# Performance work log

Hardware: AMD Instinct MI355X
Metric: run time of the kernel (lower is better)

## Reference

```python
import jax, jax.numpy as jnp
import numpy as np

N_BLOCKS = 16
BLOCK_SIZE = 512
TOP_K = N_BLOCKS // 4  # matches n_blocks // 4 in the source


def setup_inputs() -> dict:
    key = jax.random.key(0)
    k1, k2, k3, k4, k5 = jax.random.split(key, 5)
    in_f, out_f = 2048, 8192
    x = jax.random.normal(k1, (2, 4096, in_f), dtype=jnp.float32)
    # router: Linear(in_features, n_blocks)
    Wr = jax.random.normal(k2, (N_BLOCKS, in_f), dtype=jnp.float32) * (in_f ** -0.5)
    br = jnp.zeros((N_BLOCKS,), dtype=jnp.float32)
    # fc1: Linear(in, out); fc2: Linear(out, in). Biases are unused in the original forward.
    W1 = jax.random.normal(k3, (out_f, in_f), dtype=jnp.float32) * (in_f ** -0.5)
    W2 = jax.random.normal(k4, (in_f, out_f), dtype=jnp.float32) * (out_f ** -0.5)
    return {"x": x, "Wr": Wr, "br": br, "W1": W1, "W2": W2}


def reference(x, Wr, br, W1, W2):
    x_shape = x.shape
    in_f = x_shape[-1]
    xf = x.reshape(-1, in_f)                      # [N, in]
    n = xf.shape[0]
    # router + top-k block selection per token
    prob = jax.nn.softmax(xf @ Wr.T + br, axis=-1)          # [N, nb]
    _, idx = jax.lax.top_k(prob, TOP_K)                      # [N, k]
    mask = jnp.zeros((n, N_BLOCKS), dtype=xf.dtype)
    mask = mask.at[jnp.arange(n)[:, None], idx].set(1.0)     # [N, nb]
    # fc1 per block: h[n,i,b] = x @ W1_block_i^T  (bias never used in source)
    W1b = W1.reshape(N_BLOCKS, BLOCK_SIZE, in_f)
    h = jnp.einsum('nf,ibf->nib', xf, W1b)                   # [N, nb, bs]
    # activation, then zero out unselected blocks (unselected never reach fc2)
    h = jax.nn.gelu(h, approximate=False) * mask[:, :, None]
    # fc2 per block accumulate: y = sum_i h_i @ W2_block_i^T
    W2b = W2.reshape(in_f, N_BLOCKS, BLOCK_SIZE)
    y = jnp.einsum('nib,fib->nf', h, W2b)                    # [N, in]
    return y.reshape(x_shape)
```

## Files before the change

### kernel.cpp

```cpp
#include <hip/hip_runtime.h>
#include <hip/hip_bf16.h>

#define N_TOK 8192
#define IN_F  2048
#define OUT_F 8192
#define NB    16
#define BS    512
#define BM2   256
#define MAX_MT2 144

typedef short          bf16x8  __attribute__((ext_vector_type(8)));
typedef unsigned short ushort8 __attribute__((ext_vector_type(8)));
typedef float          f32x4   __attribute__((ext_vector_type(4)));
typedef _Float16       f16x8   __attribute__((ext_vector_type(8)));

#define WS_COUNTS 0
#define WS_TSTART 64
#define WS_SEL    256
#define WS_INV    (32*1024)
#define WS_LISTS  (192*1024)
#define WS_XBF    (1ull<<20)
#define WS_W2BF   WS_XBF
#define WS_H      (WS_XBF + 33554432ull)
#define WS_W1BF   (WS_H + 37748736ull)
#define WS_YP     WS_W1BF

static __device__ __forceinline__ unsigned short f2bf(float f) {
    __hip_bfloat16 h = __float2bfloat16(f);
    return *reinterpret_cast<unsigned short*>(&h);
}

static __device__ __forceinline__ void gload16(const unsigned short* g, unsigned short* lds) {
    __builtin_amdgcn_global_load_lds(
        (const __attribute__((address_space(1))) unsigned int*)g,
        (__attribute__((address_space(3))) unsigned int*)lds, 16, 0, 0);
}

__global__ __launch_bounds__(512) void router_kernel(
    const float* __restrict__ x, const float* __restrict__ Wr,
    const float* __restrict__ br, unsigned short* __restrict__ sel,
    unsigned short* __restrict__ x_bf)
{
    __shared__ float xs[8][IN_F];
    __shared__ double logits[8][NB];
    const int tid = threadIdx.x;
    const int lt = tid & 63;
    const int wv = tid >> 6;
    const int tok = blockIdx.x * 8 + wv;
    float4* xl = (float4*)xs[wv];
    const float4* xp = (const float4*)(x + (size_t)tok * IN_F);
    #pragma unroll
    for (int i = 0; i < 8; ++i) xl[lt + i * 64] = xp[lt + i * 64];
    __syncthreads();
    const int e = lt >> 2, p = lt & 3;
    const float4* wp = (const float4*)(Wr + (size_t)e * IN_F);
    double s = 0.0;
    for (int j = p; j < IN_F / 4; j += 4) {
        float4 a = xl[j], w = wp[j];
        s += (double)a.x * w.x + (double)a.y * w.y + (double)a.z * w.z + (double)a.w * w.w;
    }
    s += __shfl_down(s, 2);
    s += __shfl_down(s, 1);
    if (p == 0) logits[wv][e] = s + (double)br[e];
    __syncthreads();
    if (lt == 0) {
        unsigned used = 0, packed = 0;
        #pragma unroll
        for (int kk = 0; kk < 4; ++kk) {
            int best = 0; double bv = -1.0e300;
            #pragma unroll
            for (int i = 0; i < NB; ++i)
                if (!((used >> i) & 1u) && logits[wv][i] > bv) { bv = logits[wv][i]; best = i; }
            used |= 1u << best;
            packed |= (unsigned)best << (4 * kk);
        }
        sel[tok] = (unsigned short)packed;
    }
    const int t7 = tok & 7;
    unsigned short* drow = x_bf + (size_t)tok * IN_F;
    #pragma unroll
    for (int i = 0; i < 4; ++i) {
        const int slot = lt + i * 64;
        const float* sp = &xs[wv][slot * 8];
        ushort8 o;
        #pragma unroll
        for (int j = 0; j < 8; ++j) o[j] = f2bf(sp[j]);
        *(ushort8*)(drow + ((slot ^ t7) << 3)) = o;
    }
}

__global__ __launch_bounds__(256) void build_lists_kernel(
    const unsigned short* __restrict__ sel, int* __restrict__ counts,
    int* __restrict__ lists, unsigned* __restrict__ inv)
{
    const int e = blockIdx.x;
    const int t = threadIdx.x;
    unsigned short mysel[N_TOK / 256];
    int cnt = 0;
    #pragma unroll
    for (int i = 0; i < N_TOK / 256; ++i) {
        unsigned s = sel[i * 256 + t];
        mysel[i] = (unsigned short)s;
        bool m = ((s & 15u) == (unsigned)e) | (((s >> 4) & 15u) == (unsigned)e) |
                 (((s >> 8) & 15u) == (unsigned)e) | (((s >> 12) & 15u) == (unsigned)e);
        cnt += m ? 1 : 0;
    }
    __shared__ int ps[256];
    ps[t] = cnt;
    __syncthreads();
    #pragma unroll
    for (int off = 1; off < 256; off <<= 1) {
        int v = (t >= off) ? ps[t - off] : 0;
        __syncthreads();
        ps[t] += v;
        __syncthreads();
    }
    int pos = ps[t] - cnt;
    if (t == 255) counts[e] = ps[255];
    #pragma unroll
    for (int i = 0; i < N_TOK / 256; ++i) {
        unsigned s = mysel[i];
        bool m = ((s & 15u) == (unsigned)e) | (((s >> 4) & 15u) == (unsigned)e) |
                 (((s >> 8) & 15u) == (unsigned)e) | (((s >> 12) & 15u) == (unsigned)e);
        if (m) {
            const int tok = i * 256 + t;
            int j = ((s & 15u) == (unsigned)e) ? 0 :
                    (((s >> 4) & 15u) == (unsigned)e) ? 1 :
                    (((s >> 8) & 15u) == (unsigned)e) ? 2 : 3;
            inv[tok * 4 + j] = ((unsigned)e << 16) | (unsigned)pos;
            lists[e * N_TOK + pos++] = tok;
        }
    }
}

__global__ void scan_kernel(const int* __restrict__ counts, int* __restrict__ tstart)
{
    if (threadIdx.x == 0) {
        int acc = 0;
        for (int i = 0; i < NB; ++i) { tstart[i] = acc; acc += (counts[i] + BM2 - 1) / BM2; }
        tstart[NB] = acc;
    }
}

__global__ __launch_bounds__(256) void convert_swz_kernel(
    const float* __restrict__ src, unsigned short* __restrict__ dst, int sh)
{
    const int total = 1 << 21;
    for (int id = blockIdx.x * 256 + threadIdx.x; id < total; id += 2048 * 256) {
        const int row = id >> sh;
        const int sr  = id & ((1 << sh) - 1);
        const int ps  = sr ^ (row & 7);
        const float4* s4 = (const float4*)(src + ((size_t)id << 3));
        float4 p0 = s4[0], p1 = s4[1];
        ushort8 o;
        o[0] = f2bf(p0.x); o[1] = f2bf(p0.y); o[2] = f2bf(p0.z); o[3] = f2bf(p0.w);
        o[4] = f2bf(p1.x); o[5] = f2bf(p1.y); o[6] = f2bf(p1.z); o[7] = f2bf(p1.w);
        *(ushort8*)(dst + (((size_t)(row) << sh) << 3) + ((size_t)ps << 3)) = o;
    }
}

__global__ __launch_bounds__(512) void fc1_kernel(
    const unsigned short* __restrict__ x_bf, const unsigned short* __restrict__ w1_bf,
    const int* __restrict__ lists, const int* __restrict__ counts,
    const int* __restrict__ tstart, unsigned short* __restrict__ h)
{
    __shared__ unsigned short lds[73728];
    const int bid = blockIdx.x;
    const int newid = (bid & 7) * 72 + (bid >> 3);
    const int nt = newid & 3, mt = newid >> 2;
    if (mt >= tstart[NB]) return;
    int b = 0;
    #pragma unroll
    for (int i = 1; i < NB; ++i) b += (mt >= tstart[i]);
    const int cnt  = counts[b];
    const int row0 = (mt - tstart[b]) * BM2;
    const int tid  = threadIdx.x;
    const int wave = tid >> 6, lane = tid & 63;
    const int sph = lane & 7;
    const int rbase = wave * 8 + (lane >> 3);

    const unsigned short* aS[4];
    const unsigned short* bS[2];
    #pragma unroll
    for (int i = 0; i < 4; ++i) {
        const int r = i * 64 + rbase;
        const int gr = min(row0 + r, cnt - 1);
        const int tok = lists[b * N_TOK + gr];
        aS[i] = x_bf + (size_t)tok * IN_F + ((sph ^ (r & 7) ^ (tok & 7)) << 3);
    }
    #pragma unroll
    for (int j = 0; j < 2; ++j) {
        const int r = j * 64 + rbase;
        bS[j] = w1_bf + (size_t)(b * BS + nt * 128 + r) * IN_F + (sph << 3);
    }
    const int wbase = wave * 512;

    const int lr16 = lane & 15, q = lane >> 4;
    const int wm = (wave >> 1) * 64, wn = (wave & 1) * 64;
    int offA[4], offB[4];
    #pragma unroll
    for (int i = 0; i < 4; ++i) { const int r = wm + i * 16 + lr16; offA[i] = r * 64 + ((q ^ (r & 7)) << 3); }
    #pragma unroll
    for (int j = 0; j < 4; ++j) { const int r = wn + j * 16 + lr16; offB[j] = r * 64 + ((q ^ (r & 7)) << 3); }

    f32x4 acc[4][4];
    #pragma unroll
    for (int i = 0; i < 4; ++i)
        #pragma unroll
        for (int j = 0; j < 4; ++j) acc[i][j] = (f32x4)0.0f;

#define STA1(k, buf, i) gload16(aS[i] + (size_t)(k) * 64, lds + (buf) * 24576 + (i) * 4096 + wbase)
#define STB1(k, buf, j) gload16(bS[j] + (size_t)(k) * 64, lds + (buf) * 24576 + 16384 + (j) * 4096 + wbase)

    STA1(0,0,0); STA1(0,0,1); STA1(0,0,2); STA1(0,0,3); STB1(0,0,0); STB1(0,0,1);
    STA1(1,1,0); STA1(1,1,1); STA1(1,1,2); STA1(1,1,3); STB1(1,1,0); STB1(1,1,1);
    asm volatile("s_waitcnt vmcnt(6)" ::: "memory");
    __builtin_amdgcn_s_barrier();

    const int NK = IN_F / 64;
    int cur = 0;
    for (int k = 0; k < NK; ++k) {
        const unsigned short* Ab = lds + cur * 24576;
        const unsigned short* Bb = Ab + 16384;
        const int nxt = (cur == 0) ? 2 : cur - 1;
        bf16x8 a[8], bb[8];
        #pragma unroll
        for (int i = 0; i < 4; ++i) {
            a[i]      = *(const bf16x8*)&Ab[offA[i]];
            a[4 + i]  = *(const bf16x8*)&Ab[offA[i] ^ 32];
            bb[i]     = *(const bf16x8*)&Bb[offB[i]];
            bb[4 + i] = *(const bf16x8*)&Bb[offB[i] ^ 32];
        }
        if (k + 2 < NK) {
            STA1(k + 2, nxt, 0); STA1(k + 2, nxt, 1); STA1(k + 2, nxt, 2); STA1(k + 2, nxt, 3);
            STB1(k + 2, nxt, 0); STB1(k + 2, nxt, 1);
            asm volatile("s_waitcnt vmcnt(6)" ::: "memory");
        } else if (k + 1 < NK) {
            asm volatile("s_waitcnt vmcnt(0)" ::: "memory");
        }
        __builtin_amdgcn_s_barrier();
        asm volatile("s_waitcnt lgkmcnt(0)" ::: "memory");
        __builtin_amdgcn_sched_barrier(0);
        __builtin_amdgcn_s_setprio(1);
        #pragma unroll
        for (int hf = 0; hf < 2; ++hf)
            #pragma unroll
            for (int i = 0; i < 4; ++i)
                #pragma unroll
                for (int j = 0; j < 4; ++j)
                    acc[i][j] = __builtin_amdgcn_mfma_f32_16x16x32_bf16(a[hf * 4 + i], bb[hf * 4 + j], acc[i][j], 0, 0, 0);
        __builtin_amdgcn_s_setprio(0);
        __builtin_amdgcn_sched_barrier(0);
        __builtin_amdgcn_s_barrier();
        cur = (cur == 2) ? 0 : cur + 1;
    }
    #pragma unroll
    for (int i = 0; i < 4; ++i) {
        #pragma unroll
        for (int r = 0; r < 4; ++r) {
            const int lrow = wm + i * 16 + q * 4 + r;
            if (row0 + lrow < cnt) {
                const size_t hrow = (size_t)(mt * BM2 + lrow) * BS;
                const int r7 = (lrow & 7) << 3;
                #pragma unroll
                for (int j = 0; j < 4; ++j) {
                    const int col = nt * 128 + wn + j * 16 + lr16;
                    float v = acc[i][j][r];
                    v = 0.5f * v * (1.0f + erff(v * 0.70710678118654752f));
                    h[hrow + (col ^ r7)] = f2bf(v);
                }
            }
        }
    }
#undef STA1
#undef STB1
}

__global__ __launch_bounds__(512) void fc2_kernel(
    const unsigned short* __restrict__ h, const unsigned short* __restrict__ w2_bf,
    const int* __restrict__ counts, const int* __restrict__ tstart,
    _Float16* __restrict__ yp)
{
    __shared__ unsigned short lds[2][32768];
    const int bid = blockIdx.x;
    const int newid = (bid & 7) * 144 + (bid >> 3);
    const int nt = newid & 7, mt = newid >> 3;
    if (mt >= tstart[NB]) return;
    int b = 0;
    #pragma unroll
    for (int i = 1; i < NB; ++i) b += (mt >= tstart[i]);
    const int cnt  = counts[b];
    const int row0 = (mt - tstart[b]) * BM2;
    const int tid  = threadIdx.x;
    const int wave = tid >> 6, lane = tid & 63;
    const int sph = lane & 7;
    const int rbase = wave * 8 + (lane >> 3);

    const unsigned short* aS[4];
    const unsigned short* bS[4];
    #pragma unroll
    for (int g = 0; g < 4; ++g) {
        const int r = g * 64 + rbase;
        aS[g] = h + (size_t)(mt * BM2 + r) * BS + (sph << 3);
        bS[g] = w2_bf + (size_t)(nt * 256 + r) * OUT_F + b * BS + (sph << 3);
    }
    const int wbase = wave * 512;

    const int lr16 = lane & 15, q = lane >> 4;
    const int wr = (wave >> 2) * 128, wc = (wave & 3) * 64;
    int offA[8], offB[4];
    #pragma unroll
    for (int i = 0; i < 8; ++i) { const int r = wr + i * 16 + lr16; offA[i] = r * 64 + ((q ^ (r & 7)) << 3); }
    #pragma unroll
    for (int j = 0; j < 4; ++j) { const int r = wc + j * 16 + lr16; offB[j] = 16384 + r * 64 + ((q ^ (r & 7)) << 3); }

    f32x4 acc[8][4];
    #pragma unroll
    for (int i = 0; i < 8; ++i)
        #pragma unroll
        for (int j = 0; j < 4; ++j) acc[i][j] = (f32x4)0.0f;

#define ST2(k, buf) \
    { _Pragma("unroll") for (int g = 0; g < 4; ++g) \
        gload16(aS[g] + (size_t)(k) * 64, &lds[buf][g * 4096 + wbase]); \
      _Pragma("unroll") for (int g = 0; g < 4; ++g) \
        gload16(bS[g] + (size_t)(k) * 64, &lds[buf][16384 + g * 4096 + wbase]); }

#define MFMA_8x4 \
    __builtin_amdgcn_s_barrier(); \
    asm volatile("s_waitcnt lgkmcnt(0)" ::: "memory"); \
    __builtin_amdgcn_sched_barrier(0); \
    __builtin_amdgcn_s_setprio(1); \
    _Pragma("unroll") for (int i = 0; i < 8; ++i) \
        _Pragma("unroll") for (int j = 0; j < 4; ++j) \
            acc[i][j] = __builtin_amdgcn_mfma_f32_16x16x32_bf16(a[i], bb[j], acc[i][j], 0, 0, 0); \
    __builtin_amdgcn_s_setprio(0); \
    __builtin_amdgcn_sched_barrier(0); \
    __builtin_amdgcn_s_barrier();

    ST2(0, 0);
    asm volatile("s_waitcnt vmcnt(0)" ::: "memory");
    __builtin_amdgcn_s_barrier();

    const int NK = BS / 64;
    for (int k = 0; k < NK; ++k) {
        const int cur = k & 1;
        const unsigned short* L = lds[cur];
        {
            bf16x8 a[8], bb[4];
            #pragma unroll
            for (int i = 0; i < 8; ++i) a[i]  = *(const bf16x8*)&L[offA[i]];
            #pragma unroll
            for (int j = 0; j < 4; ++j) bb[j] = *(const bf16x8*)&L[offB[j]];
            if (k + 1 < NK) ST2(k + 1, cur ^ 1);
            MFMA_8x4
        }
        {
            bf16x8 a[8], bb[4];
            #pragma unroll
            for (int i = 0; i < 8; ++i) a[i]  = *(const bf16x8*)&L[offA[i] ^ 32];
            #pragma unroll
            for (int j = 0; j < 4; ++j) bb[j] = *(const bf16x8*)&L[offB[j] ^ 32];
            if (k + 1 < NK) asm volatile("s_waitcnt vmcnt(0)" ::: "memory");
            MFMA_8x4
        }
    }
    #pragma unroll
    for (int i = 0; i < 8; ++i) {
        #pragma unroll
        for (int r = 0; r < 4; ++r) {
            const int lrow = wr + i * 16 + q * 4 + r;
            if (row0 + lrow < cnt) {
                _Float16* yrow = yp + (size_t)(mt * BM2 + lrow) * IN_F + nt * 256 + wc + lr16;
                #pragma unroll
                for (int j = 0; j < 4; ++j)
                    yrow[j * 16] = (_Float16)acc[i][j][r];
            }
        }
    }
#undef ST2
#undef MFMA_8x4
}

__global__ __launch_bounds__(256) void reduce_kernel(
    const _Float16* __restrict__ yp, const unsigned* __restrict__ inv,
    const int* __restrict__ tstart, float* __restrict__ y)
{
    const int tok = blockIdx.x;
    __shared__ size_t rbase[4];
    if (threadIdx.x < 4) {
        unsigned v = inv[tok * 4 + threadIdx.x];
        rbase[threadIdx.x] = (size_t)(tstart[v >> 16] * BM2 + (int)(v & 0xFFFFu)) * IN_F;
    }
    __syncthreads();
    const int c = threadIdx.x * 8;
    f16x8 v0 = *(const f16x8*)(yp + rbase[0] + c);
    f16x8 v1 = *(const f16x8*)(yp + rbase[1] + c);
    f16x8 v2 = *(const f16x8*)(yp + rbase[2] + c);
    f16x8 v3 = *(const f16x8*)(yp + rbase[3] + c);
    float out[8];
    #pragma unroll
    for (int j = 0; j < 8; ++j)
        out[j] = (float)v0[j] + (float)v1[j] + (float)v2[j] + (float)v3[j];
    float4* yo = (float4*)(y + (size_t)tok * IN_F + c);
    yo[0] = make_float4(out[0], out[1], out[2], out[3]);
    yo[1] = make_float4(out[4], out[5], out[6], out[7]);
}

extern "C" void kernel_launch(void* const* d_in, const int* in_sizes, int n_in,
                              void* d_out, int out_size, void* d_ws, size_t ws_size,
                              hipStream_t stream) {
    const float* x  = (const float*)d_in[0];
    const float* Wr = (const float*)d_in[1];
    const float* br = (const float*)d_in[2];
    const float* W1 = (const float*)d_in[3];
    const float* W2 = (const float*)d_in[4];
    float* y = (float*)d_out;
    char* ws = (char*)d_ws;
    int* counts = (int*)(ws + WS_COUNTS);
    int* tstart = (int*)(ws + WS_TSTART);
    unsigned short* sel = (unsigned short*)(ws + WS_SEL);
    unsigned* inv = (unsigned*)(ws + WS_INV);
    int* lists  = (int*)(ws + WS_LISTS);
    unsigned short* x_bf  = (unsigned short*)(ws + WS_XBF);
    unsigned short* w1_bf = (unsigned short*)(ws + WS_W1BF);
    unsigned short* w2_bf = (unsigned short*)(ws + WS_W2BF);
    unsigned short* h     = (unsigned short*)(ws + WS_H);
    _Float16* yp          = (_Float16*)(ws + WS_YP);

    hipLaunchKernelGGL(router_kernel, dim3(N_TOK / 8), dim3(512), 0, stream, x, Wr, br, sel, x_bf);
    hipLaunchKernelGGL(build_lists_kernel, dim3(NB), dim3(256), 0, stream, sel, counts, lists, inv);
    hipLaunchKernelGGL(scan_kernel, dim3(1), dim3(64), 0, stream, counts, tstart);
    hipLaunchKernelGGL(convert_swz_kernel, dim3(2048), dim3(256), 0, stream, W1, w1_bf, 8);
    hipLaunchKernelGGL(fc1_kernel, dim3(4 * MAX_MT2), dim3(512), 0, stream, x_bf, w1_bf, lists, counts, tstart, h);
    hipLaunchKernelGGL(convert_swz_kernel, dim3(2048), dim3(256), 0, stream, W2, w2_bf, 10);
    hipLaunchKernelGGL(fc2_kernel, dim3(8 * MAX_MT2), dim3(512), 0, stream, h, w2_bf, counts, tstart, yp);
    hipLaunchKernelGGL(reduce_kernel, dim3(N_TOK), dim3(256), 0, stream, yp, inv, tstart, y);
}
```

Measured before the change: 398.9 us.

## Halve fc1 K-tile to 32 and shrink LDS for higher occupancy

The fc1 GEMM now stages K in chunks of 32 instead of 64, which halves the triple-buffered LDS footprint. The launch bounds now request more resident blocks per CU. The x and W1 swizzle patterns switch from 8-way to 4-way XOR to fit the narrower 64-byte rows, and the router and converter kernels are updated to match. This doubles the number of K iterations and barriers per tile in exchange for more concurrent workgroups to hide latency, and it risks more LDS bank conflicts under the weaker swizzle.

```diff
diff --git a/kernel.cpp b/kernel.cpp
--- a/kernel.cpp
+++ b/kernel.cpp
@@ -76,7 +76,7 @@
         }
         sel[tok] = (unsigned short)packed;
     }
-    const int t7 = tok & 7;
+    const int t3 = tok & 3;
     unsigned short* drow = x_bf + (size_t)tok * IN_F;
     #pragma unroll
     for (int i = 0; i < 4; ++i) {
@@ -85,7 +85,7 @@
         ushort8 o;
         #pragma unroll
         for (int j = 0; j < 8; ++j) o[j] = f2bf(sp[j]);
-        *(ushort8*)(drow + ((slot ^ t7) << 3)) = o;
+        *(ushort8*)(drow + ((slot ^ t3) << 3)) = o;
     }
 }
 
@@ -143,13 +143,13 @@
 }
 
 __global__ __launch_bounds__(256) void convert_swz_kernel(
-    const float* __restrict__ src, unsigned short* __restrict__ dst, int sh)
+    const float* __restrict__ src, unsigned short* __restrict__ dst, int sh, int mask)
 {
     const int total = 1 << 21;
     for (int id = blockIdx.x * 256 + threadIdx.x; id < total; id += 2048 * 256) {
         const int row = id >> sh;
         const int sr  = id & ((1 << sh) - 1);
-        const int ps  = sr ^ (row & 7);
+        const int ps  = sr ^ (row & mask);
         const float4* s4 = (const float4*)(src + ((size_t)id << 3));
         float4 p0 = s4[0], p1 = s4[1];
         ushort8 o;
@@ -159,12 +159,12 @@
     }
 }
 
-__global__ __launch_bounds__(512) void fc1_kernel(
+__global__ __launch_bounds__(512, 4) void fc1_kernel(
     const unsigned short* __restrict__ x_bf, const unsigned short* __restrict__ w1_bf,
     const int* __restrict__ lists, const int* __restrict__ counts,
     const int* __restrict__ tstart, unsigned short* __restrict__ h)
 {
-    __shared__ unsigned short lds[73728];
+    __shared__ unsigned short lds[36864];
     const int bid = blockIdx.x;
     const int newid = (bid & 7) * 72 + (bid >> 3);
     const int nt = newid & 3, mt = newid >> 2;
@@ -176,32 +176,29 @@
     const int row0 = (mt - tstart[b]) * BM2;
     const int tid  = threadIdx.x;
     const int wave = tid >> 6, lane = tid & 63;
-    const int sph = lane & 7;
-    const int rbase = wave * 8 + (lane >> 3);
-
-    const unsigned short* aS[4];
-    const unsigned short* bS[2];
-    #pragma unroll
-    for (int i = 0; i < 4; ++i) {
-        const int r = i * 64 + rbase;
-        const int gr = min(row0 + r, cnt - 1);
-        const int tok = lists[b * N_TOK + gr];
-        aS[i] = x_bf + (size_t)tok * IN_F + ((sph ^ (r & 7) ^ (tok & 7)) << 3);
-    }
-    #pragma unroll
-    for (int j = 0; j < 2; ++j) {
-        const int r = j * 64 + rbase;
-        bS[j] = w1_bf + (size_t)(b * BS + nt * 128 + r) * IN_F + (sph << 3);
-    }
-    const int wbase = wave * 512;
+    const int sl = tid & 3;
+    const int srw = tid >> 2;
+
+    const unsigned short* aS0;
+    const unsigned short* aS1;
+    const unsigned short* bS0;
+    {
+        int gr = min(row0 + srw, cnt - 1);
+        int tok = lists[b * N_TOK + gr];
+        aS0 = x_bf + (size_t)tok * IN_F + ((sl ^ (srw & 3) ^ (tok & 3)) << 3);
+        gr = min(row0 + srw + 128, cnt - 1);
+        tok = lists[b * N_TOK + gr];
+        aS1 = x_bf + (size_t)tok * IN_F + ((sl ^ ((srw + 128) & 3) ^ (tok & 3)) << 3);
+        bS0 = w1_bf + (size_t)(b * BS + nt * 128 + srw) * IN_F + (sl << 3);
+    }
 
     const int lr16 = lane & 15, q = lane >> 4;
     const int wm = (wave >> 1) * 64, wn = (wave & 1) * 64;
     int offA[4], offB[4];
     #pragma unroll
-    for (int i = 0; i < 4; ++i) { const int r = wm + i * 16 + lr16; offA[i] = r * 64 + ((q ^ (r & 7)) << 3); }
-    #pragma unroll
-    for (int j = 0; j < 4; ++j) { const int r = wn + j * 16 + lr16; offB[j] = r * 64 + ((q ^ (r & 7)) << 3); }
+    for (int i = 0; i < 4; ++i) { const int r = wm + i * 16 + lr16; offA[i] = r * 32 + ((q ^ (r & 3)) << 3); }
+    #pragma unroll
+    for (int j = 0; j < 4; ++j) { const int r = wn + j * 16 + lr16; offB[j] = 8192 + r * 32 + ((q ^ (r & 3)) << 3); }
 
     f32x4 acc[4][4];
     #pragma unroll
@@ -209,32 +206,29 @@
         #pragma unroll
         for (int j = 0; j < 4; ++j) acc[i][j] = (f32x4)0.0f;
 
-#define STA1(k, buf, i) gload16(aS[i] + (size_t)(k) * 64, lds + (buf) * 24576 + (i) * 4096 + wbase)
-#define STB1(k, buf, j) gload16(bS[j] + (size_t)(k) * 64, lds + (buf) * 24576 + 16384 + (j) * 4096 + wbase)
-
-    STA1(0,0,0); STA1(0,0,1); STA1(0,0,2); STA1(0,0,3); STB1(0,0,0); STB1(0,0,1);
-    STA1(1,1,0); STA1(1,1,1); STA1(1,1,2); STA1(1,1,3); STB1(1,1,0); STB1(1,1,1);
-    asm volatile("s_waitcnt vmcnt(6)" ::: "memory");
+#define ST1(k, buf) \
+    { gload16(aS0 + (size_t)(k) * 32, lds + (buf) * 12288 + tid * 8); \
+      gload16(aS1 + (size_t)(k) * 32, lds + (buf) * 12288 + 4096 + tid * 8); \
+      gload16(bS0 + (size_t)(k) * 32, lds + (buf) * 12288 + 8192 + tid * 8); }
+
+    ST1(0, 0); ST1(1, 1);
+    asm volatile("s_waitcnt vmcnt(3)" ::: "memory");
     __builtin_amdgcn_s_barrier();
 
-    const int NK = IN_F / 64;
+    const int NK = IN_F / 32;
     int cur = 0;
     for (int k = 0; k < NK; ++k) {
-        const unsigned short* Ab = lds + cur * 24576;
-        const unsigned short* Bb = Ab + 16384;
+        const unsigned short* L = lds + cur * 12288;
         const int nxt = (cur == 0) ? 2 : cur - 1;
-        bf16x8 a[8], bb[8];
+        bf16x8 a[4], bb[4];
         #pragma unroll
         for (int i = 0; i < 4; ++i) {
-            a[i]      = *(const bf16x8*)&Ab[offA[i]];
-            a[4 + i]  = *(const bf16x8*)&Ab[offA[i] ^ 32];
-            bb[i]     = *(const bf16x8*)&Bb[offB[i]];
-            bb[4 + i] = *(const bf16x8*)&Bb[offB[i] ^ 32];
+            a[i]  = *(const bf16x8*)&L[offA[i]];
+            bb[i] = *(const bf16x8*)&L[offB[i]];
         }
         if (k + 2 < NK) {
-            STA1(k + 2, nxt, 0); STA1(k + 2, nxt, 1); STA1(k + 2, nxt, 2); STA1(k + 2, nxt, 3);
-            STB1(k + 2, nxt, 0); STB1(k + 2, nxt, 1);
-            asm volatile("s_waitcnt vmcnt(6)" ::: "memory");
+            ST1(k + 2, nxt);
+            asm volatile("s_waitcnt vmcnt(3)" ::: "memory");
         } else if (k + 1 < NK) {
             asm volatile("s_waitcnt vmcnt(0)" ::: "memory");
         }
@@ -243,12 +237,10 @@
         __builtin_amdgcn_sched_barrier(0);
         __builtin_amdgcn_s_setprio(1);
         #pragma unroll
-        for (int hf = 0; hf < 2; ++hf)
-            #pragma unroll
-            for (int i = 0; i < 4; ++i)
-                #pragma unroll
-                for (int j = 0; j < 4; ++j)
-                    acc[i][j] = __builtin_amdgcn_mfma_f32_16x16x32_bf16(a[hf * 4 + i], bb[hf * 4 + j], acc[i][j], 0, 0, 0);
+        for (int i = 0; i < 4; ++i)
+            #pragma unroll
+            for (int j = 0; j < 4; ++j)
+                acc[i][j] = __builtin_amdgcn_mfma_f32_16x16x32_bf16(a[i], bb[j], acc[i][j], 0, 0, 0);
         __builtin_amdgcn_s_setprio(0);
         __builtin_amdgcn_sched_barrier(0);
         __builtin_amdgcn_s_barrier();
@@ -272,8 +264,7 @@
             }
         }
     }
-#undef STA1
-#undef STB1
+#undef ST1
 }
 
 __global__ __launch_bounds__(512) void fc2_kernel(
@@ -431,9 +422,9 @@
     hipLaunchKernelGGL(router_kernel, dim3(N_TOK / 8), dim3(512), 0, stream, x, Wr, br, sel, x_bf);
     hipLaunchKernelGGL(build_lists_kernel, dim3(NB), dim3(256), 0, stream, sel, counts, lists, inv);
     hipLaunchKernelGGL(scan_kernel, dim3(1), dim3(64), 0, stream, counts, tstart);
-    hipLaunchKernelGGL(convert_swz_kernel, dim3(2048), dim3(256), 0, stream, W1, w1_bf, 8);
+    hipLaunchKernelGGL(convert_swz_kernel, dim3(2048), dim3(256), 0, stream, W1, w1_bf, 8, 3);
     hipLaunchKernelGGL(fc1_kernel, dim3(4 * MAX_MT2), dim3(512), 0, stream, x_bf, w1_bf, lists, counts, tstart, h);
-    hipLaunchKernelGGL(convert_swz_kernel, dim3(2048), dim3(256), 0, stream, W2, w2_bf, 10);
+    hipLaunchKernelGGL(convert_swz_kernel, dim3(2048), dim3(256), 0, stream, W2, w2_bf, 10, 7);
     hipLaunchKernelGGL(fc2_kernel, dim3(8 * MAX_MT2), dim3(512), 0, stream, h, w2_bf, counts, tstart, yp);
     hipLaunchKernelGGL(reduce_kernel, dim3(N_TOK), dim3(256), 0, stream, yp, inv, tstart, y);
 }
```

New measurement: 398.5 us. About the same (-0.1%).
